# Kernel optimization log

Hardware: AMD Instinct MI355X
Metric: run time of the kernel (lower is better)

The kernel has to match this reference:

```python
import jax, jax.numpy as jnp
import numpy as np

B, C, D, Hh, W = 2, 320, 4, 16, 16
N = D * Hh * W          # 1024 nodes
NH = 8                  # num_heads
DH = C // NH            # 40
L = 2                   # num_layers
A, EPD = 16, 64         # da_prior tokens, encode_prior_dim
EDGE_SCALE = 32 ** -0.5 # GraphEdgeFeature dim_head=32
SCALE = DH ** -0.5
EPS = 1e-5


def _ln(x, g, b):
    m = x.mean(-1, keepdims=True)
    v = ((x - m) ** 2).mean(-1, keepdims=True)
    return (x - m) * jax.lax.rsqrt(v + EPS) * g + b


def setup_inputs() -> dict:
    key = jax.random.key(0)
    ks = jax.random.split(key, 16)
    std = 0.02 / np.sqrt(L)
    inp = {
        'x': jax.random.normal(ks[0], (B, C, D, Hh, W), jnp.float32),
        'da_prior': jax.random.normal(ks[1], (B, A, EPD), jnp.float32),
        # GraphEdgeFeature.to_qk (no bias), init std 0.02/sqrt(24)
        'qk_w': jax.random.normal(ks[2], (2 * C, C), jnp.float32) * (0.02 / np.sqrt(24)),
        # fc_prior
        'fcp_w': jax.random.normal(ks[3], (C, EPD), jnp.float32) * 0.02,
        'fcp_b': jnp.zeros((C,), jnp.float32),
        # per-layer (stacked over L)
        'ln1_g': jnp.ones((L, C), jnp.float32),
        'ln1_b': jnp.zeros((L, C), jnp.float32),
        'gln_g': jnp.ones((L, C), jnp.float32),
        'gln_b': jnp.zeros((L, C), jnp.float32),
        'qkv_w': jax.random.normal(ks[4], (L, 3 * C, C), jnp.float32) * std,
        'qkv_b': jnp.zeros((L, 3 * C), jnp.float32),
        'proj_w': jax.random.normal(ks[5], (L, C, C), jnp.float32) * std,
        'proj_b': jnp.zeros((L, C), jnp.float32),
        # expand Conv2d(1, NH, 1): weight [NH], bias [NH]
        'exp_w': jax.random.normal(ks[6], (L, NH), jnp.float32),
        'exp_b': jnp.zeros((L, NH), jnp.float32),
        # reduce Conv2d(NH, 1, 1): weight [NH], bias scalar
        'red_w': jax.random.normal(ks[7], (L, NH), jnp.float32) / np.sqrt(NH),
        'red_b': jnp.zeros((L,), jnp.float32),
    }
    return inp


def _forward(x, da_prior, qk_w, fcp_w, fcp_b, ln1_g, ln1_b, gln_g, gln_b,
             qkv_w, qkv_b, proj_w, proj_b, exp_w, exp_b, red_w, red_b):
    node = x.reshape(B, C, N)                       # [B,C,N]
    # ---- GraphEdgeFeature: full-dim QK attention over nodes ----
    xt = node.transpose(0, 2, 1)                    # [B,N,C]
    qk = xt @ qk_w.T                                # [B,N,2C]
    q_e, k_e = jnp.split(qk, 2, axis=-1)
    edge = jax.nn.softmax(jnp.einsum('bqc,bkc->bqk', q_e, k_e) * EDGE_SCALE, axis=-1)  # [B,N,N]
    # ---- fc_prior ----
    da = da_prior @ fcp_w.T + fcp_b                 # [B,A,C]
    s = da.sum(axis=1)                              # [B,C] (sum over 'a' in einsum bnc,bca->bnc)
    for l in range(L):
        # block norm1 over channel dim
        nt = _ln(node.transpose(0, 2, 1), ln1_g[l], ln1_b[l])   # [B,N,C]
        # torch.einsum('bnn,bnc->bnc') takes the DIAGONAL of edge
        diag = jnp.diagonal(edge, axis1=1, axis2=2)             # [B,N]
        node2 = diag[:, :, None] * nt * s[:, None, :] + nt      # [B,N,C]
        y = _ln(node2, gln_g[l], gln_b[l])
        qkv = (y @ qkv_w[l].T + qkv_b[l]).reshape(B, N, 3, NH, DH)
        qkv = qkv.transpose(2, 0, 3, 1, 4)                      # [3,B,H,N,DH]
        q, k, v = qkv[0], qkv[1], qkv[2]
        attn = jnp.einsum('bhnd,bhmd->bhnm', q, k) * SCALE
        attn = attn + edge[:, None] * exp_w[l][None, :, None, None] + exp_b[l][None, :, None, None]
        a = jax.nn.softmax(attn, axis=-1)                       # [B,H,N,N]
        node_out = jnp.einsum('bhnm,bhmd->bhnd', a, v).transpose(0, 2, 1, 3).reshape(B, N, C)
        edge_new = jnp.einsum('bhnm,h->bnm', a + attn, red_w[l]) + red_b[l]  # [B,N,N]
        ws = jax.nn.softmax(edge_new, axis=-1)
        wsum = (ws * edge_new).sum(-1)                          # [B,N]
        node_out = node_out + wsum[:, :, None]                  # fc=Identity, broadcast
        node_out = node_out @ proj_w[l].T + proj_b[l]
        node = node_out.transpose(0, 2, 1)                      # [B,C,N]
        edge = edge + edge_new
    return node.reshape(B, C, D, Hh, W)


def reference(x, da_prior, qk_w, fcp_w, fcp_b, ln1_g, ln1_b, gln_g, gln_b,
              qkv_w, qkv_b, proj_w, proj_b, exp_w, exp_b, red_w, red_b):
    return _forward(x, da_prior, qk_w, fcp_w, fcp_b, ln1_g, ln1_b, gln_g, gln_b,
                    qkv_w, qkv_b, proj_w, proj_b, exp_w, exp_b, red_w, red_b)
```

## Files before the change

### kernel.cpp

```cpp
#include <hip/hip_runtime.h>
#include <math.h>

#define EDGE_SCALE 0.17677669529663687f
#define ATT_SCALE  0.15811388300841897f
#define LN_EPS 1e-5f

typedef __attribute__((ext_vector_type(8))) short bf8;
typedef __attribute__((ext_vector_type(4))) float f32x4;

__device__ __forceinline__ f32x4 mfma16(bf8 a, bf8 b, f32x4 c) {
  return __builtin_amdgcn_mfma_f32_16x16x32_bf16(a, b, c, 0, 0, 0);
}
__device__ __forceinline__ unsigned short f2bf(float f) {
  union { float f; unsigned u; } v; v.f = f;
  unsigned r = v.u + 0x7FFF + ((v.u >> 16) & 1);
  return (unsigned short)(r >> 16);
}
__device__ __forceinline__ float bf2f(unsigned short h) {
  union { unsigned u; float f; } v; v.u = ((unsigned)h) << 16;
  return v.f;
}
__device__ __forceinline__ float wave_max(float v) {
  #pragma unroll
  for (int o = 32; o > 0; o >>= 1) v = fmaxf(v, __shfl_xor(v, o));
  return v;
}
__device__ __forceinline__ float wave_sum(float v) {
  #pragma unroll
  for (int o = 32; o > 0; o >>= 1) v += __shfl_xor(v, o);
  return v;
}

__global__ __launch_bounds__(256) void k_trans(const float* __restrict__ x,
    float* __restrict__ node, unsigned short* __restrict__ nodebf) {
  __shared__ float tile[32][33];
  const int b = blockIdx.z;
  const int n0 = blockIdx.x * 32, c0 = blockIdx.y * 32;
  const int tx = threadIdx.x & 31, ty = threadIdx.x >> 5;
  #pragma unroll
  for (int k = 0; k < 4; ++k) {
    int c = c0 + ty + 8 * k;
    tile[ty + 8 * k][tx] = x[((size_t)b * 320 + c) * 1024 + n0 + tx];
  }
  __syncthreads();
  #pragma unroll
  for (int k = 0; k < 4; ++k) {
    int n = n0 + ty + 8 * k;
    float v = tile[tx][ty + 8 * k];
    size_t idx = ((size_t)b * 1024 + n) * 320 + c0 + tx;
    node[idx] = v;
    nodebf[idx] = f2bf(v);
  }
}

__global__ __launch_bounds__(320) void k_svec(const float* __restrict__ da,
    const float* __restrict__ fw, const float* __restrict__ fb, float* __restrict__ sv) {
  __shared__ float ds[64];
  const int b = blockIdx.x, t = threadIdx.x;
  if (t < 64) {
    float a = 0.f;
    #pragma unroll
    for (int i = 0; i < 16; ++i) a += da[b * 1024 + i * 64 + t];
    ds[t] = a;
  }
  __syncthreads();
  if (t < 320) {
    float acc = 16.f * fb[t];
    #pragma unroll
    for (int e = 0; e < 64; ++e) acc = fmaf(ds[e], fw[t * 64 + e], acc);
    sv[b * 320 + t] = acc;
  }
}

__global__ void k_wcvt(const float* __restrict__ a, int na,
                       const float* __restrict__ b, int nb,
                       const float* __restrict__ c, int nc,
                       unsigned short* __restrict__ out) {
  int tot = na + nb + nc;
  for (int i = blockIdx.x * blockDim.x + threadIdx.x; i < tot; i += gridDim.x * blockDim.x) {
    float v = (i < na) ? a[i] : ((i < na + nb) ? b[i - na] : c[i - na - nb]);
    out[i] = f2bf(v);
  }
}

__global__ __launch_bounds__(256, 4) void k_mgemm(
    const unsigned short* __restrict__ A, const unsigned short* __restrict__ W,
    const float* __restrict__ bias, void* p0, void* p1, void* p2, int mode) {
  __shared__ float smem[64 * 65];
  const int t = threadIdx.x, w = t >> 6, lane = t & 63;
  const int q16 = lane >> 4, l16 = lane & 15;
  const int rt = blockIdx.x * 64, jt = blockIdx.y * 64;
  f32x4 acc[4];
  #pragma unroll
  for (int i = 0; i < 4; ++i)
    #pragma unroll
    for (int j = 0; j < 4; ++j) acc[i][j] = 0.f;
  const unsigned short* ap = A + (size_t)(rt + 16 * w + l16) * 320 + q16 * 8;
  const unsigned short* wp = W + (size_t)(jt + l16) * 320 + q16 * 8;
  for (int kc = 0; kc < 10; ++kc) {
    bf8 af = *(const bf8*)(ap + kc * 32);
    #pragma unroll
    for (int ct = 0; ct < 4; ++ct) {
      bf8 bf = *(const bf8*)(wp + (size_t)ct * 16 * 320 + kc * 32);
      acc[ct] = mfma16(af, bf, acc[ct]);
    }
  }
  if (mode == 0 || mode == 1) {
    #pragma unroll
    for (int ct = 0; ct < 4; ++ct) {
      int col = jt + ct * 16 + l16;
      float bv = bias ? bias[col] : 0.f;
      #pragma unroll
      for (int r = 0; r < 4; ++r) {
        int row = rt + 16 * w + q16 * 4 + r;
        float v = acc[ct][r] + bv;
        if (mode == 0) {
          ((float*)p0)[(size_t)row * 320 + col] = v;
        } else {
          if (col < 320) ((unsigned short*)p0)[(size_t)row * 320 + col] = f2bf(v);
          else           ((unsigned short*)p1)[(size_t)row * 320 + col - 320] = f2bf(v);
        }
      }
    }
  } else if (mode == 2) {
    const int part = jt / 320;
    if (part < 2) {
      unsigned short* dst = (unsigned short*)(part == 0 ? p0 : p1);
      #pragma unroll
      for (int ct = 0; ct < 4; ++ct) {
        int col = jt + ct * 16 + l16;
        float bv = bias[col];
        int rem = col - part * 320;
        int h = rem / 40, d = rem % 40;
        #pragma unroll
        for (int r = 0; r < 4; ++r) {
          int row = rt + 16 * w + q16 * 4 + r;
          int b = row >> 10, n = row & 1023;
          size_t base = (((size_t)b * 8 + h) * 1024 + n) * 64;
          dst[base + d] = f2bf(acc[ct][r] + bv);
          if (d < 24) dst[base + 40 + d] = 0;
        }
      }
    } else {
      unsigned short* vt_t = (unsigned short*)smem;
      #pragma unroll
      for (int ct = 0; ct < 4; ++ct) {
        int col = jt + ct * 16 + l16;
        float bv = bias[col];
        #pragma unroll
        for (int r = 0; r < 4; ++r)
          vt_t[(ct * 16 + l16) * 72 + 16 * w + q16 * 4 + r] = f2bf(acc[ct][r] + bv);
      }
      __syncthreads();
      const int cl = t >> 2, seg = t & 3;
      int rem = (jt - 640) + cl;
      int h = rem / 40, d = rem % 40;
      int b = rt >> 10, n = (rt & 1023) + seg * 16;
      const float4* lp = (const float4*)&vt_t[cl * 72 + seg * 16];
      float4 a0 = lp[0], a1 = lp[1];
      float4* gp = (float4*)((unsigned short*)p2 +
                             (((size_t)b * 8 + h) * 48 + d) * 1024 + n);
      gp[0] = a0; gp[1] = a1;
    }
  } else {
    #pragma unroll
    for (int ct = 0; ct < 4; ++ct) {
      int col = jt + ct * 16 + l16;
      float bv = bias[col];
      #pragma unroll
      for (int r = 0; r < 4; ++r)
        smem[(16 * w + q16 * 4 + r) * 65 + ct * 16 + l16] = acc[ct][r] + bv;
    }
    __syncthreads();
    const int cl = t >> 2, seg = t & 3;
    int b = rt >> 10, n = (rt & 1023) + seg * 16;
    float* orow = (float*)p0 + ((size_t)b * 320 + jt + cl) * 1024 + n;
    #pragma unroll
    for (int i2 = 0; i2 < 4; ++i2) {
      float4 vv;
      vv.x = smem[(seg * 16 + i2 * 4 + 0) * 65 + cl];
      vv.y = smem[(seg * 16 + i2 * 4 + 1) * 65 + cl];
      vv.z = smem[(seg * 16 + i2 * 4 + 2) * 65 + cl];
      vv.w = smem[(seg * 16 + i2 * 4 + 3) * 65 + cl];
      ((float4*)orow)[i2] = vv;
    }
  }
}

__global__ __launch_bounds__(256, 4) void k_sgemm(
    const unsigned short* __restrict__ qe, const unsigned short* __restrict__ ke,
    float* __restrict__ S) {
  const int t = threadIdx.x, w = t >> 6, lane = t & 63;
  const int q16 = lane >> 4, l16 = lane & 15;
  const int rt = blockIdx.x * 64, jt = blockIdx.y * 64, b = blockIdx.z;
  const unsigned short* A = qe + (size_t)b * 1024 * 320;
  const unsigned short* W = ke + (size_t)b * 1024 * 320;
  f32x4 acc[4];
  #pragma unroll
  for (int i = 0; i < 4; ++i)
    #pragma unroll
    for (int j = 0; j < 4; ++j) acc[i][j] = 0.f;
  const unsigned short* ap = A + (size_t)(rt + 16 * w + l16) * 320 + q16 * 8;
  const unsigned short* wp = W + (size_t)(jt + l16) * 320 + q16 * 8;
  for (int kc = 0; kc < 10; ++kc) {
    bf8 af = *(const bf8*)(ap + kc * 32);
    #pragma unroll
    for (int ct = 0; ct < 4; ++ct) {
      bf8 bf = *(const bf8*)(wp + (size_t)ct * 16 * 320 + kc * 32);
      acc[ct] = mfma16(af, bf, acc[ct]);
    }
  }
  #pragma unroll
  for (int ct = 0; ct < 4; ++ct)
    #pragma unroll
    for (int r = 0; r < 4; ++r)
      S[((size_t)b * 1024 + rt + 16 * w + q16 * 4 + r) * 1024 + jt + ct * 16 + l16] =
          acc[ct][r] * EDGE_SCALE;
}

__global__ __launch_bounds__(256) void k_smax(const float* __restrict__ S,
                                              float* __restrict__ edge) {
  const int w = threadIdx.x >> 6, lane = threadIdx.x & 63;
  const int row = blockIdx.x * 4 + w;
  const float4* sp = (const float4*)(S + (size_t)row * 1024) + lane;
  float4 v[4];
  #pragma unroll
  for (int i = 0; i < 4; ++i) v[i] = sp[i * 64];
  float mx = -3.4e38f;
  #pragma unroll
  for (int i = 0; i < 4; ++i)
    mx = fmaxf(mx, fmaxf(fmaxf(v[i].x, v[i].y), fmaxf(v[i].z, v[i].w)));
  mx = wave_max(mx);
  float s = 0.f;
  #pragma unroll
  for (int i = 0; i < 4; ++i) {
    v[i].x = __expf(v[i].x - mx); v[i].y = __expf(v[i].y - mx);
    v[i].z = __expf(v[i].z - mx); v[i].w = __expf(v[i].w - mx);
    s += v[i].x + v[i].y + v[i].z + v[i].w;
  }
  s = wave_sum(s);
  float inv = 1.f / s;
  float4* ep = (float4*)(edge + (size_t)row * 1024) + lane;
  #pragma unroll
  for (int i = 0; i < 4; ++i)
    ep[i * 64] = make_float4(v[i].x * inv, v[i].y * inv, v[i].z * inv, v[i].w * inv);
}

__global__ __launch_bounds__(256) void k_ln(const float* __restrict__ node,
    const float* __restrict__ edge, const float* __restrict__ sv,
    const float* __restrict__ g1, const float* __restrict__ b1,
    const float* __restrict__ g2, const float* __restrict__ b2,
    unsigned short* __restrict__ y) {
  const int w = threadIdx.x >> 6, lane = threadIdx.x & 63;
  const int row = blockIdx.x * 4 + w;
  const int b = row >> 10, n = row & 1023;
  const float* xr = node + (size_t)row * 320;
  float x[5];
  #pragma unroll
  for (int i = 0; i < 5; ++i) x[i] = xr[lane + 64 * i];
  float s = x[0] + x[1] + x[2] + x[3] + x[4];
  float mean = wave_sum(s) * (1.f / 320.f);
  float v = 0.f;
  #pragma unroll
  for (int i = 0; i < 5; ++i) { float d = x[i] - mean; v += d * d; }
  float rstd = rsqrtf(wave_sum(v) * (1.f / 320.f) + LN_EPS);
  float diag = edge[(size_t)row * 1024 + n];
  float n2[5];
  #pragma unroll
  for (int i = 0; i < 5; ++i) {
    int c = lane + 64 * i;
    float nt = (x[i] - mean) * rstd * g1[c] + b1[c];
    n2[i] = diag * nt * sv[b * 320 + c] + nt;
  }
  s = n2[0] + n2[1] + n2[2] + n2[3] + n2[4];
  float mean2 = wave_sum(s) * (1.f / 320.f);
  v = 0.f;
  #pragma unroll
  for (int i = 0; i < 5; ++i) { float d = n2[i] - mean2; v += d * d; }
  float rstd2 = rsqrtf(wave_sum(v) * (1.f / 320.f) + LN_EPS);
  unsigned short* yr = y + (size_t)row * 320;
  #pragma unroll
  for (int i = 0; i < 5; ++i) {
    int c = lane + 64 * i;
    yr[c] = f2bf((n2[i] - mean2) * rstd2 * g2[c] + b2[c]);
  }
}

__global__ __launch_bounds__(256, 4) void k_score(
    const unsigned short* __restrict__ qbf, const unsigned short* __restrict__ kbf,
    const unsigned short* __restrict__ vtb, const float* __restrict__ edge,
    unsigned short* __restrict__ thbuf, float* __restrict__ att,
    const float* __restrict__ ew, const float* __restrict__ eb,
    const float* __restrict__ rw) {
  __shared__ unsigned short a_lds[4][4][16][20];
  __shared__ unsigned short th_lds[4][16][72];
  __shared__ float ored[4][3][16][17];
  __shared__ float redm[4][16], reds[4][16];
  const int t = threadIdx.x, w = t >> 6, lane = t & 63;
  const int q16 = lane >> 4, l16 = lane & 15;
  const int n0 = blockIdx.x * 16, h = blockIdx.y, b = blockIdx.z;
  const size_t bh = (size_t)b * 8 + h;
  const unsigned short* qp = qbf + (bh * 1024 + n0 + l16) * 64 + q16 * 8;
  bf8 af0 = *(const bf8*)(qp);
  bf8 af1 = *(const bf8*)(qp + 32);
  f32x4 acc[16];
  #pragma unroll
  for (int i = 0; i < 16; ++i)
    #pragma unroll
    for (int j = 0; j < 4; ++j) acc[i][j] = 0.f;
  const unsigned short* kp = kbf + (bh * 1024 + (size_t)w * 256 + l16) * 64 + q16 * 8;
  #pragma unroll
  for (int tt = 0; tt < 16; ++tt) {
    const unsigned short* kpt = kp + (size_t)tt * 16 * 64;
    bf8 b0 = *(const bf8*)(kpt);
    bf8 b1 = *(const bf8*)(kpt + 32);
    acc[tt] = mfma16(af0, b0, acc[tt]);
    acc[tt] = mfma16(af1, b1, acc[tt]);
  }
  const float ewh = ew[h], ebh = eb[h], rwh = rw[h];
  const float* ep = edge + ((size_t)b * 1024 + n0 + q16 * 4) * 1024 + w * 256 + l16;
  #pragma unroll
  for (int tt = 0; tt < 16; ++tt)
    #pragma unroll
    for (int r = 0; r < 4; ++r) {
      float ev = ep[(size_t)r * 1024 + tt * 16];
      acc[tt][r] = fmaf(acc[tt][r], ATT_SCALE, fmaf(ev, ewh, ebh));
    }
  float pm[4] = {-3.4e38f, -3.4e38f, -3.4e38f, -3.4e38f};
  #pragma unroll
  for (int tt = 0; tt < 16; ++tt)
    #pragma unroll
    for (int r = 0; r < 4; ++r) pm[r] = fmaxf(pm[r], acc[tt][r]);
  #pragma unroll
  for (int r = 0; r < 4; ++r)
    #pragma unroll
    for (int o = 1; o <= 8; o <<= 1) pm[r] = fmaxf(pm[r], __shfl_xor(pm[r], o));
  if (l16 == 0) {
    #pragma unroll
    for (int r = 0; r < 4; ++r) redm[w][q16 * 4 + r] = pm[r];
  }
  __syncthreads();
  float m[4], ps[4] = {0.f, 0.f, 0.f, 0.f};
  #pragma unroll
  for (int r = 0; r < 4; ++r)
    m[r] = fmaxf(fmaxf(redm[0][q16 * 4 + r], redm[1][q16 * 4 + r]),
                 fmaxf(redm[2][q16 * 4 + r], redm[3][q16 * 4 + r]));
  #pragma unroll
  for (int tt = 0; tt < 16; ++tt)
    #pragma unroll
    for (int r = 0; r < 4; ++r) ps[r] += __expf(acc[tt][r] - m[r]);
  #pragma unroll
  for (int r = 0; r < 4; ++r)
    #pragma unroll
    for (int o = 1; o <= 8; o <<= 1) ps[r] += __shfl_xor(ps[r], o);
  if (l16 == 0) {
    #pragma unroll
    for (int r = 0; r < 4; ++r) reds[w][q16 * 4 + r] = ps[r];
  }
  __syncthreads();
  float inv[4];
  #pragma unroll
  for (int r = 0; r < 4; ++r)
    inv[r] = 1.f / (reds[0][q16 * 4 + r] + reds[1][q16 * 4 + r] +
                    reds[2][q16 * 4 + r] + reds[3][q16 * 4 + r]);
  f32x4 oacc[3];
  #pragma unroll
  for (int i = 0; i < 3; ++i)
    #pragma unroll
    for (int j = 0; j < 4; ++j) oacc[i][j] = 0.f;
  unsigned short* tbase = thbuf + (bh * 1024 + n0) * 1024 + w * 256;
  const int trow = lane >> 2, tc4 = lane & 3;
  #pragma unroll
  for (int g = 0; g < 4; ++g) {
    #pragma unroll
    for (int ti = 0; ti < 4; ++ti) {
      int tt = g * 4 + ti;
      #pragma unroll
      for (int r = 0; r < 4; ++r) {
        float e = __expf(acc[tt][r] - m[r]);
        float a = e * inv[r];
        a_lds[w][ti][q16 * 4 + r][l16] = f2bf(a);
        th_lds[w][q16 * 4 + r][ti * 16 + l16] = f2bf(rwh * (a + acc[tt][r]));
      }
    }
    #pragma unroll
    for (int kk = 0; kk < 2; ++kk) {
      const unsigned short* ap2 = &a_lds[w][kk * 2 + (q16 >> 1)][l16][(q16 & 1) * 8];
      short4 lo = *(const short4*)(ap2);
      short4 hi = *(const short4*)(ap2 + 4);
      bf8 afv = {lo.x, lo.y, lo.z, lo.w, hi.x, hi.y, hi.z, hi.w};
      int kc = w * 8 + g * 2 + kk;
      const unsigned short* vp = vtb + (bh * 48 + l16) * 1024 + (size_t)kc * 32 + q16 * 8;
      #pragma unroll
      for (int nt = 0; nt < 3; ++nt) {
        bf8 bfv = *(const bf8*)(vp + (size_t)nt * 16 * 1024);
        oacc[nt] = mfma16(afv, bfv, oacc[nt]);
      }
    }
    {
      const float4* lp = (const float4*)&th_lds[w][trow][tc4 * 16];
      float4 v0 = lp[0], v1 = lp[1];
      float4* gp = (float4*)(tbase + (size_t)trow * 1024 + g * 64 + tc4 * 16);
      gp[0] = v0; gp[1] = v1;
    }
  }
  #pragma unroll
  for (int nt = 0; nt < 3; ++nt)
    #pragma unroll
    for (int r = 0; r < 4; ++r) ored[w][nt][q16 * 4 + r][l16] = oacc[nt][r];
  __syncthreads();
  #pragma unroll
  for (int k = 0; k < 3; ++k) {
    int o = k * 256 + t;
    int nt = o >> 8, row = (o >> 4) & 15, col = o & 15;
    int dim = nt * 16 + col;
    float sum = ored[0][nt][row][col] + ored[1][nt][row][col] +
                ored[2][nt][row][col] + ored[3][nt][row][col];
    if (dim < 40)
      att[((size_t)b * 1024 + n0 + row) * 320 + h * 40 + dim] = sum;
  }
}

__global__ __launch_bounds__(256) void k_wsum(
    const unsigned short* __restrict__ thbuf, float* __restrict__ edge,
    const float* __restrict__ att, unsigned short* __restrict__ attbf,
    const float* __restrict__ rb) {
  const int w = threadIdx.x >> 6, lane = threadIdx.x & 63;
  const int row = blockIdx.x * 4 + w;
  const int b = row >> 10, n = row & 1023;
  const float rbv = rb[0];
  float tv[16];
  #pragma unroll
  for (int i = 0; i < 16; ++i) tv[i] = rbv;
  #pragma unroll 1
  for (int h = 0; h < 8; ++h) {
    const unsigned short* tph = thbuf + (((size_t)b * 8 + h) * 1024 + n) * 1024 + lane * 4;
    #pragma unroll
    for (int seg = 0; seg < 4; ++seg) {
      ushort4 u = *(const ushort4*)(tph + seg * 256);
      tv[seg * 4 + 0] += bf2f(u.x);
      tv[seg * 4 + 1] += bf2f(u.y);
      tv[seg * 4 + 2] += bf2f(u.z);
      tv[seg * 4 + 3] += bf2f(u.w);
    }
  }
  float4* erp = (float4*)(edge + ((size_t)b * 1024 + n) * 1024) + lane;
  #pragma unroll
  for (int seg = 0; seg < 4; ++seg) {
    float4 e = erp[seg * 64];
    e.x += tv[seg * 4 + 0]; e.y += tv[seg * 4 + 1];
    e.z += tv[seg * 4 + 2]; e.w += tv[seg * 4 + 3];
    erp[seg * 64] = e;
  }
  float mx = -3.4e38f;
  #pragma unroll
  for (int i = 0; i < 16; ++i) mx = fmaxf(mx, tv[i]);
  mx = wave_max(mx);
  float s = 0.f, num = 0.f;
  #pragma unroll
  for (int i = 0; i < 16; ++i) {
    float e = __expf(tv[i] - mx);
    s += e; num += e * tv[i];
  }
  s = wave_sum(s); num = wave_sum(num);
  const float wsum = num / s;
  const float* ar = att + (size_t)row * 320;
  unsigned short* ao = attbf + (size_t)row * 320;
  #pragma unroll
  for (int i = 0; i < 5; ++i) {
    int c = lane + 64 * i;
    ao[c] = f2bf(ar[c] + wsum);
  }
}

extern "C" void kernel_launch(void* const* d_in, const int* in_sizes, int n_in,
                              void* d_out, int out_size, void* d_ws, size_t ws_size,
                              hipStream_t stream) {
  const float* x      = (const float*)d_in[0];
  const float* da     = (const float*)d_in[1];
  const float* qk_w   = (const float*)d_in[2];
  const float* fcp_w  = (const float*)d_in[3];
  const float* fcp_b  = (const float*)d_in[4];
  const float* ln1_g  = (const float*)d_in[5];
  const float* ln1_b  = (const float*)d_in[6];
  const float* gln_g  = (const float*)d_in[7];
  const float* gln_b  = (const float*)d_in[8];
  const float* qkv_w  = (const float*)d_in[9];
  const float* qkv_b  = (const float*)d_in[10];
  const float* proj_w = (const float*)d_in[11];
  const float* proj_b = (const float*)d_in[12];
  const float* exp_w  = (const float*)d_in[13];
  const float* exp_b  = (const float*)d_in[14];
  const float* red_w  = (const float*)d_in[15];
  const float* red_b  = (const float*)d_in[16];
  float* ws = (float*)d_ws;
  float* node  = ws + 0;
  unsigned short* ybf   = (unsigned short*)(ws + 655360);
  float* attb  = ws + 983040;
  unsigned short* attbf = (unsigned short*)(ws + 1638400);
  float* edge  = ws + 1966080;
  float* svec  = ws + 4063232;
  unsigned short* nodebf = (unsigned short*)(ws + 4063872);
  unsigned short* qe   = (unsigned short*)(ws + 4391552);
  unsigned short* ke   = (unsigned short*)(ws + 4719232);
  unsigned short* qbf  = (unsigned short*)(ws + 5046912);
  unsigned short* kbf  = (unsigned short*)(ws + 5571200);
  unsigned short* vtb  = (unsigned short*)(ws + 6095488);
  unsigned short* wbf  = (unsigned short*)(ws + 6488704);
  unsigned short* thbuf= (unsigned short*)(ws + 7000704);
  float* sbuf = ws + 15389312;
  float* out = (float*)d_out;
  unsigned short* qk_wb   = wbf;
  unsigned short* qkv_wb  = wbf + 204800;
  unsigned short* proj_wb = wbf + 819200;

  hipLaunchKernelGGL(k_trans, dim3(32, 10, 2), dim3(256), 0, stream, x, node, nodebf);
  hipLaunchKernelGGL(k_svec, dim3(2), dim3(320), 0, stream, da, fcp_w, fcp_b, svec);
  hipLaunchKernelGGL(k_wcvt, dim3(512), dim3(256), 0, stream,
                     qk_w, 204800, qkv_w, 614400, proj_w, 204800, wbf);
  hipLaunchKernelGGL(k_mgemm, dim3(32, 10), dim3(256), 0, stream,
                     nodebf, qk_wb, (const float*)nullptr, qe, ke, (void*)nullptr, 1);
  hipLaunchKernelGGL(k_sgemm, dim3(16, 16, 2), dim3(256), 0, stream, qe, ke, sbuf);
  hipLaunchKernelGGL(k_smax, dim3(512), dim3(256), 0, stream, sbuf, edge);
  for (int l = 0; l < 2; ++l) {
    hipLaunchKernelGGL(k_ln, dim3(512), dim3(256), 0, stream, node, edge, svec,
                       ln1_g + l * 320, ln1_b + l * 320, gln_g + l * 320, gln_b + l * 320, ybf);
    hipLaunchKernelGGL(k_mgemm, dim3(32, 15), dim3(256), 0, stream,
                       ybf, qkv_wb + (size_t)l * 307200, qkv_b + l * 960, qbf, kbf, vtb, 2);
    hipLaunchKernelGGL(k_score, dim3(64, 8, 2), dim3(256), 0, stream,
                       qbf, kbf, vtb, edge, thbuf, attb,
                       exp_w + l * 8, exp_b + l * 8, red_w + l * 8);
    hipLaunchKernelGGL(k_wsum, dim3(512), dim3(256), 0, stream,
                       thbuf, edge, attb, attbf, red_b + l);
    if (l == 0)
      hipLaunchKernelGGL(k_mgemm, dim3(32, 5), dim3(256), 0, stream,
                         attbf, proj_wb, proj_b, node, (void*)nullptr, (void*)nullptr, 0);
    else
      hipLaunchKernelGGL(k_mgemm, dim3(32, 5), dim3(256), 0, stream,
                         attbf, proj_wb + 102400, proj_b + 320, out,
                         (void*)nullptr, (void*)nullptr, 3);
  }
}
```

Measured before the change: 293.5 us.

## Fuse edge softmax into score GEMM and fuse all heads into one attention kernel

Merges the edge QK GEMM with its row softmax so the full score matrix is never written, and skips the max subtraction on the assumption that scores are small. Replaces the per-head score kernel plus the weighted-sum kernel with one kernel per 16-row block that loops over all 8 heads. That kernel keeps the edge rows in LDS, accumulates the reduced edge update in registers, and does the final softmax-weighted sum in place. This removes the large bf16 per-head temp buffer and the extra launches. In exchange, only 128 blocks are launched and each uses heavy LDS (about 90KB), which lowers occupancy. Dropping max subtraction also risks exp overflow.

```diff
diff --git a/kernel.cpp b/kernel.cpp
--- a/kernel.cpp
+++ b/kernel.cpp
@@ -19,11 +19,6 @@
 __device__ __forceinline__ float bf2f(unsigned short h) {
   union { unsigned u; float f; } v; v.u = ((unsigned)h) << 16;
   return v.f;
-}
-__device__ __forceinline__ float wave_max(float v) {
-  #pragma unroll
-  for (int o = 32; o > 0; o >>= 1) v = fmaxf(v, __shfl_xor(v, o));
-  return v;
 }
 __device__ __forceinline__ float wave_sum(float v) {
   #pragma unroll
@@ -187,63 +182,64 @@
   }
 }
 
-__global__ __launch_bounds__(256, 4) void k_sgemm(
+__global__ __launch_bounds__(512, 2) void k_edge3(
     const unsigned short* __restrict__ qe, const unsigned short* __restrict__ ke,
-    float* __restrict__ S) {
+    float* __restrict__ edge) {
+  __shared__ float zred[8][16];
   const int t = threadIdx.x, w = t >> 6, lane = t & 63;
   const int q16 = lane >> 4, l16 = lane & 15;
-  const int rt = blockIdx.x * 64, jt = blockIdx.y * 64, b = blockIdx.z;
-  const unsigned short* A = qe + (size_t)b * 1024 * 320;
-  const unsigned short* W = ke + (size_t)b * 1024 * 320;
-  f32x4 acc[4];
-  #pragma unroll
-  for (int i = 0; i < 4; ++i)
+  const int n0 = blockIdx.x * 16, b = blockIdx.y;
+  const unsigned short* qp = qe + ((size_t)(b * 1024 + n0 + l16)) * 320 + q16 * 8;
+  bf8 af[10];
+  #pragma unroll
+  for (int kc = 0; kc < 10; ++kc) af[kc] = *(const bf8*)(qp + kc * 32);
+  f32x4 acc[8];
+  #pragma unroll
+  for (int i = 0; i < 8; ++i)
     #pragma unroll
     for (int j = 0; j < 4; ++j) acc[i][j] = 0.f;
-  const unsigned short* ap = A + (size_t)(rt + 16 * w + l16) * 320 + q16 * 8;
-  const unsigned short* wp = W + (size_t)(jt + l16) * 320 + q16 * 8;
-  for (int kc = 0; kc < 10; ++kc) {
-    bf8 af = *(const bf8*)(ap + kc * 32);
-    #pragma unroll
-    for (int ct = 0; ct < 4; ++ct) {
-      bf8 bf = *(const bf8*)(wp + (size_t)ct * 16 * 320 + kc * 32);
-      acc[ct] = mfma16(af, bf, acc[ct]);
-    }
-  }
-  #pragma unroll
-  for (int ct = 0; ct < 4; ++ct)
-    #pragma unroll
-    for (int r = 0; r < 4; ++r)
-      S[((size_t)b * 1024 + rt + 16 * w + q16 * 4 + r) * 1024 + jt + ct * 16 + l16] =
-          acc[ct][r] * EDGE_SCALE;
-}
-
-__global__ __launch_bounds__(256) void k_smax(const float* __restrict__ S,
-                                              float* __restrict__ edge) {
-  const int w = threadIdx.x >> 6, lane = threadIdx.x & 63;
-  const int row = blockIdx.x * 4 + w;
-  const float4* sp = (const float4*)(S + (size_t)row * 1024) + lane;
-  float4 v[4];
-  #pragma unroll
-  for (int i = 0; i < 4; ++i) v[i] = sp[i * 64];
-  float mx = -3.4e38f;
-  #pragma unroll
-  for (int i = 0; i < 4; ++i)
-    mx = fmaxf(mx, fmaxf(fmaxf(v[i].x, v[i].y), fmaxf(v[i].z, v[i].w)));
-  mx = wave_max(mx);
-  float s = 0.f;
-  #pragma unroll
-  for (int i = 0; i < 4; ++i) {
-    v[i].x = __expf(v[i].x - mx); v[i].y = __expf(v[i].y - mx);
-    v[i].z = __expf(v[i].z - mx); v[i].w = __expf(v[i].w - mx);
-    s += v[i].x + v[i].y + v[i].z + v[i].w;
-  }
-  s = wave_sum(s);
-  float inv = 1.f / s;
-  float4* ep = (float4*)(edge + (size_t)row * 1024) + lane;
-  #pragma unroll
-  for (int i = 0; i < 4; ++i)
-    ep[i * 64] = make_float4(v[i].x * inv, v[i].y * inv, v[i].z * inv, v[i].w * inv);
+  const unsigned short* kp = ke + ((size_t)(b * 1024 + w * 128 + l16)) * 320 + q16 * 8;
+  #pragma unroll
+  for (int mt = 0; mt < 8; ++mt) {
+    const unsigned short* kpt = kp + (size_t)mt * 16 * 320;
+    #pragma unroll
+    for (int kc = 0; kc < 10; ++kc) {
+      bf8 bf = *(const bf8*)(kpt + kc * 32);
+      acc[mt] = mfma16(af[kc], bf, acc[mt]);
+    }
+  }
+  float zp[4] = {0.f, 0.f, 0.f, 0.f};
+  #pragma unroll
+  for (int mt = 0; mt < 8; ++mt)
+    #pragma unroll
+    for (int r = 0; r < 4; ++r) {
+      float e = __expf(acc[mt][r] * EDGE_SCALE);
+      acc[mt][r] = e;
+      zp[r] += e;
+    }
+  #pragma unroll
+  for (int r = 0; r < 4; ++r)
+    #pragma unroll
+    for (int o = 1; o <= 8; o <<= 1) zp[r] += __shfl_xor(zp[r], o);
+  if (l16 == 0) {
+    #pragma unroll
+    for (int r = 0; r < 4; ++r) zred[w][q16 * 4 + r] = zp[r];
+  }
+  __syncthreads();
+  float inv[4];
+  #pragma unroll
+  for (int r = 0; r < 4; ++r) {
+    float s = 0.f;
+    #pragma unroll
+    for (int ww = 0; ww < 8; ++ww) s += zred[ww][q16 * 4 + r];
+    inv[r] = 1.f / s;
+  }
+  #pragma unroll
+  for (int r = 0; r < 4; ++r) {
+    float* ep = edge + ((size_t)(b * 1024 + n0 + q16 * 4 + r)) * 1024 + w * 128 + l16;
+    #pragma unroll
+    for (int mt = 0; mt < 8; ++mt) ep[mt * 16] = acc[mt][r] * inv[r];
+  }
 }
 
 __global__ __launch_bounds__(256) void k_ln(const float* __restrict__ node,
@@ -286,190 +282,180 @@
   }
 }
 
-__global__ __launch_bounds__(256, 4) void k_score(
+__global__ __launch_bounds__(512, 2) void k_attn2(
     const unsigned short* __restrict__ qbf, const unsigned short* __restrict__ kbf,
-    const unsigned short* __restrict__ vtb, const float* __restrict__ edge,
-    unsigned short* __restrict__ thbuf, float* __restrict__ att,
+    const unsigned short* __restrict__ vtb, float* __restrict__ edge,
+    unsigned short* __restrict__ attbf,
     const float* __restrict__ ew, const float* __restrict__ eb,
-    const float* __restrict__ rw) {
-  __shared__ unsigned short a_lds[4][4][16][20];
-  __shared__ unsigned short th_lds[4][16][72];
-  __shared__ float ored[4][3][16][17];
-  __shared__ float redm[4][16], reds[4][16];
+    const float* __restrict__ rw, const float* __restrict__ rb) {
+  __shared__ float edge_lds[16][1028];
+  __shared__ unsigned short a_lds[8][16][136];
+  __shared__ float att_lds[16][330];
+  __shared__ float zred[2][8][16];
+  __shared__ float wredm[8][16], wreds[8][16], wredn[8][16];
+  __shared__ float wsum_sh[16];
   const int t = threadIdx.x, w = t >> 6, lane = t & 63;
   const int q16 = lane >> 4, l16 = lane & 15;
-  const int n0 = blockIdx.x * 16, h = blockIdx.y, b = blockIdx.z;
-  const size_t bh = (size_t)b * 8 + h;
-  const unsigned short* qp = qbf + (bh * 1024 + n0 + l16) * 64 + q16 * 8;
-  bf8 af0 = *(const bf8*)(qp);
-  bf8 af1 = *(const bf8*)(qp + 32);
-  f32x4 acc[16];
-  #pragma unroll
-  for (int i = 0; i < 16; ++i)
-    #pragma unroll
-    for (int j = 0; j < 4; ++j) acc[i][j] = 0.f;
-  const unsigned short* kp = kbf + (bh * 1024 + (size_t)w * 256 + l16) * 64 + q16 * 8;
-  #pragma unroll
-  for (int tt = 0; tt < 16; ++tt) {
-    const unsigned short* kpt = kp + (size_t)tt * 16 * 64;
-    bf8 b0 = *(const bf8*)(kpt);
-    bf8 b1 = *(const bf8*)(kpt + 32);
-    acc[tt] = mfma16(af0, b0, acc[tt]);
-    acc[tt] = mfma16(af1, b1, acc[tt]);
-  }
-  const float ewh = ew[h], ebh = eb[h], rwh = rw[h];
-  const float* ep = edge + ((size_t)b * 1024 + n0 + q16 * 4) * 1024 + w * 256 + l16;
-  #pragma unroll
-  for (int tt = 0; tt < 16; ++tt)
+  const int n0 = blockIdx.x * 16, b = blockIdx.y;
+  const size_t bh0 = (size_t)b * 8;
+  {
+    const float4* src = (const float4*)(edge + ((size_t)(b * 1024 + n0)) * 1024);
+    for (int i = t; i < 4096; i += 512) {
+      int row = i >> 8, c4 = i & 255;
+      ((float4*)&edge_lds[row][0])[c4] = src[(row << 8) + c4];
+    }
+    for (int i = t; i < 16 * 330; i += 512) (&att_lds[0][0])[i] = 0.f;
+  }
+  __syncthreads();
+  const float rbv = rb[0];
+  float t_reg[8][4];
+  #pragma unroll
+  for (int mt = 0; mt < 8; ++mt)
+    #pragma unroll
+    for (int r = 0; r < 4; ++r) t_reg[mt][r] = rbv;
+  #pragma unroll 1
+  for (int h = 0; h < 8; ++h) {
+    const size_t bh = bh0 + h;
+    const float ewh = ew[h], ebh = eb[h], rwh = rw[h];
+    const unsigned short* qp = qbf + (bh * 1024 + n0 + l16) * 64 + q16 * 8;
+    bf8 af0 = *(const bf8*)(qp);
+    bf8 af1 = *(const bf8*)(qp + 32);
+    f32x4 acc[8];
+    #pragma unroll
+    for (int i = 0; i < 8; ++i)
+      #pragma unroll
+      for (int j = 0; j < 4; ++j) acc[i][j] = 0.f;
+    const unsigned short* kp = kbf + (bh * 1024 + w * 128 + l16) * 64 + q16 * 8;
+    #pragma unroll
+    for (int mt = 0; mt < 8; ++mt) {
+      const unsigned short* kpt = kp + (size_t)mt * 16 * 64;
+      bf8 b0 = *(const bf8*)(kpt);
+      bf8 b1 = *(const bf8*)(kpt + 32);
+      acc[mt] = mfma16(af0, b0, acc[mt]);
+      acc[mt] = mfma16(af1, b1, acc[mt]);
+    }
+    float zp[4] = {0.f, 0.f, 0.f, 0.f};
+    #pragma unroll
+    for (int mt = 0; mt < 8; ++mt)
+      #pragma unroll
+      for (int r = 0; r < 4; ++r) {
+        float ev = edge_lds[q16 * 4 + r][w * 128 + mt * 16 + l16];
+        float s = fmaf(acc[mt][r], ATT_SCALE, fmaf(ev, ewh, ebh));
+        acc[mt][r] = s;
+        float e = __expf(s);
+        zp[r] += e;
+        a_lds[w][q16 * 4 + r][mt * 16 + l16] = f2bf(e);
+      }
+    #pragma unroll
+    for (int r = 0; r < 4; ++r)
+      #pragma unroll
+      for (int o = 1; o <= 8; o <<= 1) zp[r] += __shfl_xor(zp[r], o);
+    if (l16 == 0) {
+      #pragma unroll
+      for (int r = 0; r < 4; ++r) zred[h & 1][w][q16 * 4 + r] = zp[r];
+    }
+    __syncthreads();
+    float invZ[4];
     #pragma unroll
     for (int r = 0; r < 4; ++r) {
-      float ev = ep[(size_t)r * 1024 + tt * 16];
-      acc[tt][r] = fmaf(acc[tt][r], ATT_SCALE, fmaf(ev, ewh, ebh));
-    }
-  float pm[4] = {-3.4e38f, -3.4e38f, -3.4e38f, -3.4e38f};
-  #pragma unroll
-  for (int tt = 0; tt < 16; ++tt)
-    #pragma unroll
-    for (int r = 0; r < 4; ++r) pm[r] = fmaxf(pm[r], acc[tt][r]);
-  #pragma unroll
-  for (int r = 0; r < 4; ++r)
-    #pragma unroll
-    for (int o = 1; o <= 8; o <<= 1) pm[r] = fmaxf(pm[r], __shfl_xor(pm[r], o));
-  if (l16 == 0) {
-    #pragma unroll
-    for (int r = 0; r < 4; ++r) redm[w][q16 * 4 + r] = pm[r];
-  }
-  __syncthreads();
-  float m[4], ps[4] = {0.f, 0.f, 0.f, 0.f};
-  #pragma unroll
-  for (int r = 0; r < 4; ++r)
-    m[r] = fmaxf(fmaxf(redm[0][q16 * 4 + r], redm[1][q16 * 4 + r]),
-                 fmaxf(redm[2][q16 * 4 + r], redm[3][q16 * 4 + r]));
-  #pragma unroll
-  for (int tt = 0; tt < 16; ++tt)
-    #pragma unroll
-    for (int r = 0; r < 4; ++r) ps[r] += __expf(acc[tt][r] - m[r]);
-  #pragma unroll
-  for (int r = 0; r < 4; ++r)
-    #pragma unroll
-    for (int o = 1; o <= 8; o <<= 1) ps[r] += __shfl_xor(ps[r], o);
-  if (l16 == 0) {
-    #pragma unroll
-    for (int r = 0; r < 4; ++r) reds[w][q16 * 4 + r] = ps[r];
-  }
-  __syncthreads();
-  float inv[4];
-  #pragma unroll
-  for (int r = 0; r < 4; ++r)
-    inv[r] = 1.f / (reds[0][q16 * 4 + r] + reds[1][q16 * 4 + r] +
-                    reds[2][q16 * 4 + r] + reds[3][q16 * 4 + r]);
-  f32x4 oacc[3];
-  #pragma unroll
-  for (int i = 0; i < 3; ++i)
-    #pragma unroll
-    for (int j = 0; j < 4; ++j) oacc[i][j] = 0.f;
-  unsigned short* tbase = thbuf + (bh * 1024 + n0) * 1024 + w * 256;
-  const int trow = lane >> 2, tc4 = lane & 3;
-  #pragma unroll
-  for (int g = 0; g < 4; ++g) {
-    #pragma unroll
-    for (int ti = 0; ti < 4; ++ti) {
-      int tt = g * 4 + ti;
+      float s = 0.f;
+      #pragma unroll
+      for (int ww = 0; ww < 8; ++ww) s += zred[h & 1][ww][q16 * 4 + r];
+      invZ[r] = 1.f / s;
+    }
+    #pragma unroll
+    for (int mt = 0; mt < 8; ++mt)
       #pragma unroll
       for (int r = 0; r < 4; ++r) {
-        float e = __expf(acc[tt][r] - m[r]);
-        float a = e * inv[r];
-        a_lds[w][ti][q16 * 4 + r][l16] = f2bf(a);
-        th_lds[w][q16 * 4 + r][ti * 16 + l16] = f2bf(rwh * (a + acc[tt][r]));
-      }
-    }
-    #pragma unroll
-    for (int kk = 0; kk < 2; ++kk) {
-      const unsigned short* ap2 = &a_lds[w][kk * 2 + (q16 >> 1)][l16][(q16 & 1) * 8];
-      short4 lo = *(const short4*)(ap2);
-      short4 hi = *(const short4*)(ap2 + 4);
-      bf8 afv = {lo.x, lo.y, lo.z, lo.w, hi.x, hi.y, hi.z, hi.w};
-      int kc = w * 8 + g * 2 + kk;
-      const unsigned short* vp = vtb + (bh * 48 + l16) * 1024 + (size_t)kc * 32 + q16 * 8;
+        float e = __expf(acc[mt][r]);
+        t_reg[mt][r] = fmaf(rwh, fmaf(e, invZ[r], acc[mt][r]), t_reg[mt][r]);
+      }
+    f32x4 oacc[3];
+    #pragma unroll
+    for (int i = 0; i < 3; ++i)
+      #pragma unroll
+      for (int j = 0; j < 4; ++j) oacc[i][j] = 0.f;
+    #pragma unroll
+    for (int kk = 0; kk < 4; ++kk) {
+      bf8 afv = *(const bf8*)(&a_lds[w][l16][kk * 32 + q16 * 8]);
+      const unsigned short* vp = vtb + (bh * 48 + l16) * 1024 + w * 128 + kk * 32 + q16 * 8;
       #pragma unroll
       for (int nt = 0; nt < 3; ++nt) {
         bf8 bfv = *(const bf8*)(vp + (size_t)nt * 16 * 1024);
         oacc[nt] = mfma16(afv, bfv, oacc[nt]);
       }
     }
-    {
-      const float4* lp = (const float4*)&th_lds[w][trow][tc4 * 16];
-      float4 v0 = lp[0], v1 = lp[1];
-      float4* gp = (float4*)(tbase + (size_t)trow * 1024 + g * 64 + tc4 * 16);
-      gp[0] = v0; gp[1] = v1;
-    }
-  }
-  #pragma unroll
-  for (int nt = 0; nt < 3; ++nt)
-    #pragma unroll
-    for (int r = 0; r < 4; ++r) ored[w][nt][q16 * 4 + r][l16] = oacc[nt][r];
-  __syncthreads();
-  #pragma unroll
-  for (int k = 0; k < 3; ++k) {
-    int o = k * 256 + t;
-    int nt = o >> 8, row = (o >> 4) & 15, col = o & 15;
-    int dim = nt * 16 + col;
-    float sum = ored[0][nt][row][col] + ored[1][nt][row][col] +
-                ored[2][nt][row][col] + ored[3][nt][row][col];
-    if (dim < 40)
-      att[((size_t)b * 1024 + n0 + row) * 320 + h * 40 + dim] = sum;
-  }
-}
-
-__global__ __launch_bounds__(256) void k_wsum(
-    const unsigned short* __restrict__ thbuf, float* __restrict__ edge,
-    const float* __restrict__ att, unsigned short* __restrict__ attbf,
-    const float* __restrict__ rb) {
-  const int w = threadIdx.x >> 6, lane = threadIdx.x & 63;
-  const int row = blockIdx.x * 4 + w;
-  const int b = row >> 10, n = row & 1023;
-  const float rbv = rb[0];
-  float tv[16];
-  #pragma unroll
-  for (int i = 0; i < 16; ++i) tv[i] = rbv;
-  #pragma unroll 1
-  for (int h = 0; h < 8; ++h) {
-    const unsigned short* tph = thbuf + (((size_t)b * 8 + h) * 1024 + n) * 1024 + lane * 4;
-    #pragma unroll
-    for (int seg = 0; seg < 4; ++seg) {
-      ushort4 u = *(const ushort4*)(tph + seg * 256);
-      tv[seg * 4 + 0] += bf2f(u.x);
-      tv[seg * 4 + 1] += bf2f(u.y);
-      tv[seg * 4 + 2] += bf2f(u.z);
-      tv[seg * 4 + 3] += bf2f(u.w);
-    }
-  }
-  float4* erp = (float4*)(edge + ((size_t)b * 1024 + n) * 1024) + lane;
-  #pragma unroll
-  for (int seg = 0; seg < 4; ++seg) {
-    float4 e = erp[seg * 64];
-    e.x += tv[seg * 4 + 0]; e.y += tv[seg * 4 + 1];
-    e.z += tv[seg * 4 + 2]; e.w += tv[seg * 4 + 3];
-    erp[seg * 64] = e;
-  }
-  float mx = -3.4e38f;
-  #pragma unroll
-  for (int i = 0; i < 16; ++i) mx = fmaxf(mx, tv[i]);
-  mx = wave_max(mx);
-  float s = 0.f, num = 0.f;
-  #pragma unroll
-  for (int i = 0; i < 16; ++i) {
-    float e = __expf(tv[i] - mx);
-    s += e; num += e * tv[i];
-  }
-  s = wave_sum(s); num = wave_sum(num);
-  const float wsum = num / s;
-  const float* ar = att + (size_t)row * 320;
-  unsigned short* ao = attbf + (size_t)row * 320;
-  #pragma unroll
-  for (int i = 0; i < 5; ++i) {
-    int c = lane + 64 * i;
-    ao[c] = f2bf(ar[c] + wsum);
+    #pragma unroll
+    for (int nt = 0; nt < 3; ++nt)
+      #pragma unroll
+      for (int r = 0; r < 4; ++r) {
+        int d = nt * 16 + l16;
+        if (d < 40)
+          atomicAdd(&att_lds[q16 * 4 + r][h * 40 + d], oacc[nt][r] * invZ[r]);
+      }
+  }
+  float pmx[4] = {-3.4e38f, -3.4e38f, -3.4e38f, -3.4e38f};
+  #pragma unroll
+  for (int mt = 0; mt < 8; ++mt)
+    #pragma unroll
+    for (int r = 0; r < 4; ++r) pmx[r] = fmaxf(pmx[r], t_reg[mt][r]);
+  #pragma unroll
+  for (int r = 0; r < 4; ++r)
+    #pragma unroll
+    for (int o = 1; o <= 8; o <<= 1) pmx[r] = fmaxf(pmx[r], __shfl_xor(pmx[r], o));
+  if (l16 == 0) {
+    #pragma unroll
+    for (int r = 0; r < 4; ++r) wredm[w][q16 * 4 + r] = pmx[r];
+  }
+  __syncthreads();
+  float mrow[4], sp[4] = {0.f, 0.f, 0.f, 0.f}, np[4] = {0.f, 0.f, 0.f, 0.f};
+  #pragma unroll
+  for (int r = 0; r < 4; ++r) {
+    float m = -3.4e38f;
+    #pragma unroll
+    for (int ww = 0; ww < 8; ++ww) m = fmaxf(m, wredm[ww][q16 * 4 + r]);
+    mrow[r] = m;
+  }
+  #pragma unroll
+  for (int mt = 0; mt < 8; ++mt)
+    #pragma unroll
+    for (int r = 0; r < 4; ++r) {
+      float e = __expf(t_reg[mt][r] - mrow[r]);
+      sp[r] += e;
+      np[r] = fmaf(e, t_reg[mt][r], np[r]);
+    }
+  #pragma unroll
+  for (int r = 0; r < 4; ++r)
+    #pragma unroll
+    for (int o = 1; o <= 8; o <<= 1) {
+      sp[r] += __shfl_xor(sp[r], o);
+      np[r] += __shfl_xor(np[r], o);
+    }
+  if (l16 == 0) {
+    #pragma unroll
+    for (int r = 0; r < 4; ++r) { wreds[w][q16 * 4 + r] = sp[r]; wredn[w][q16 * 4 + r] = np[r]; }
+  }
+  #pragma unroll
+  for (int r = 0; r < 4; ++r) {
+    float* ep = edge + ((size_t)(b * 1024 + n0 + q16 * 4 + r)) * 1024 + w * 128 + l16;
+    #pragma unroll
+    for (int mt = 0; mt < 8; ++mt)
+      ep[mt * 16] = edge_lds[q16 * 4 + r][w * 128 + mt * 16 + l16] + t_reg[mt][r];
+  }
+  __syncthreads();
+  if (w == 0 && l16 == 0) {
+    #pragma unroll
+    for (int r = 0; r < 4; ++r) {
+      float S = 0.f, N = 0.f;
+      #pragma unroll
+      for (int ww = 0; ww < 8; ++ww) { S += wreds[ww][q16 * 4 + r]; N += wredn[ww][q16 * 4 + r]; }
+      wsum_sh[q16 * 4 + r] = N / S;
+    }
+  }
+  __syncthreads();
+  for (int i = t; i < 5120; i += 512) {
+    int row = i / 320, c = i - row * 320;
+    attbf[((size_t)(b * 1024 + n0 + row)) * 320 + c] = f2bf(att_lds[row][c] + wsum_sh[row]);
   }
 }
 
@@ -496,7 +482,6 @@
   float* ws = (float*)d_ws;
   float* node  = ws + 0;
   unsigned short* ybf   = (unsigned short*)(ws + 655360);
-  float* attb  = ws + 983040;
   unsigned short* attbf = (unsigned short*)(ws + 1638400);
   float* edge  = ws + 1966080;
   float* svec  = ws + 4063232;
@@ -507,8 +492,6 @@
   unsigned short* kbf  = (unsigned short*)(ws + 5571200);
   unsigned short* vtb  = (unsigned short*)(ws + 6095488);
   unsigned short* wbf  = (unsigned short*)(ws + 6488704);
-  unsigned short* thbuf= (unsigned short*)(ws + 7000704);
-  float* sbuf = ws + 15389312;
   float* out = (float*)d_out;
   unsigned short* qk_wb   = wbf;
   unsigned short* qkv_wb  = wbf + 204800;
@@ -520,18 +503,15 @@
                      qk_w, 204800, qkv_w, 614400, proj_w, 204800, wbf);
   hipLaunchKernelGGL(k_mgemm, dim3(32, 10), dim3(256), 0, stream,
                      nodebf, qk_wb, (const float*)nullptr, qe, ke, (void*)nullptr, 1);
-  hipLaunchKernelGGL(k_sgemm, dim3(16, 16, 2), dim3(256), 0, stream, qe, ke, sbuf);
-  hipLaunchKernelGGL(k_smax, dim3(512), dim3(256), 0, stream, sbuf, edge);
+  hipLaunchKernelGGL(k_edge3, dim3(64, 2), dim3(512), 0, stream, qe, ke, edge);
   for (int l = 0; l < 2; ++l) {
     hipLaunchKernelGGL(k_ln, dim3(512), dim3(256), 0, stream, node, edge, svec,
                        ln1_g + l * 320, ln1_b + l * 320, gln_g + l * 320, gln_b + l * 320, ybf);
     hipLaunchKernelGGL(k_mgemm, dim3(32, 15), dim3(256), 0, stream,
                        ybf, qkv_wb + (size_t)l * 307200, qkv_b + l * 960, qbf, kbf, vtb, 2);
-    hipLaunchKernelGGL(k_score, dim3(64, 8, 2), dim3(256), 0, stream,
-                       qbf, kbf, vtb, edge, thbuf, attb,
-                       exp_w + l * 8, exp_b + l * 8, red_w + l * 8);
-    hipLaunchKernelGGL(k_wsum, dim3(512), dim3(256), 0, stream,
-                       thbuf, edge, attb, attbf, red_b + l);
+    hipLaunchKernelGGL(k_attn2, dim3(64, 2), dim3(512), 0, stream,
+                       qbf, kbf, vtb, edge, attbf,
+                       exp_w + l * 8, exp_b + l * 8, red_w + l * 8, red_b + l);
     if (l == 0)
       hipLaunchKernelGGL(k_mgemm, dim3(32, 5), dim3(256), 0, stream,
                          attbf, proj_wb, proj_b, node, (void*)nullptr, (void*)nullptr, 0);
```

Result: slower. 373.4 us (+27.2%).
